# Kernel optimization log

Measured on AMD Instinct MI355X. Metric: run time of the kernel, lower is better.

## Reference

```python
import jax, jax.numpy as jnp
import numpy as np

THETA = 0.5
LEAF_SIZE = 32
N_ATOMS = 8192
N_GRAPHS = 2


def _build_tree(pos_np, indices):
    # Mirrors OpenBoundaryTreeLongRangeKernel._build_tree (octree split at bbox center).
    local = pos_np[indices]
    cmin = local.min(axis=0)
    cmax = local.max(axis=0)
    center = 0.5 * (cmin + cmax)
    half = float((cmax - cmin).max() * 0.5)
    node = {"indices": indices, "iset": set(indices), "center": center,
            "half": half, "children": [], "cid": -1}
    if len(indices) <= LEAF_SIZE:
        return node
    bins = {}
    for i in indices:
        p = pos_np[i]
        key = (int(p[0] >= center[0]), int(p[1] >= center[1]), int(p[2] >= center[2]))
        bins.setdefault(key, []).append(i)
    if len(bins) <= 1:
        return node  # degenerate split -> treated as leaf (is_leaf == no children)
    node["children"] = [_build_tree(pos_np, ci) for ci in bins.values()]
    return node


def _plan(pos_np, batch_np, n_graphs, soft):
    # Host-side Barnes-Hut traversal (the torch original does this with .item() syncs).
    # Emits flat (target, source) direct pairs and (target, cluster) monopole pairs.
    direct_t, direct_s, clus_t, clus_c = [], [], [], []
    clusters = []
    for g in range(n_graphs):
        idx = np.nonzero(batch_np == g)[0]
        if idx.size == 0:
            continue
        root = _build_tree(pos_np, [int(i) for i in idx])
        for t in idx:
            t = int(t)
            tpos = pos_np[t]
            stack = [root]
            while stack:
                node = stack.pop()
                if not node["children"]:  # leaf: direct near-field sum
                    for s in node["indices"]:
                        if s != t:
                            direct_t.append(t)
                            direct_s.append(s)
                    continue
                d = tpos - node["center"]
                dist = float(np.sqrt((d * d).sum() + soft * soft))
                diam = max(2.0 * node["half"], 1e-9)
                if (t not in node["iset"]) and (diam / dist < THETA):
                    if node["cid"] < 0:
                        node["cid"] = len(clusters)
                        clusters.append(node["indices"])
                    clus_t.append(t)
                    clus_c.append(node["cid"])
                else:
                    stack.extend(node["children"])
    if clusters:
        midx = np.concatenate([np.asarray(c, dtype=np.int32) for c in clusters])
        mseg = np.concatenate([np.full(len(c), i, np.int32) for i, c in enumerate(clusters)])
        mcnt = np.asarray([len(c) for c in clusters], dtype=np.float32)
    else:
        midx = np.zeros((0,), np.int32)
        mseg = np.zeros((0,), np.int32)
        mcnt = np.ones((1,), np.float32)
    return (np.asarray(direct_t, np.int32), np.asarray(direct_s, np.int32),
            np.asarray(clus_t, np.int32), np.asarray(clus_c, np.int32),
            midx, mseg, mcnt, max(len(clusters), 1))


def _energy(pos, source, screening, softening, plan, n_atoms):
    # Vectorized, differentiable evaluation of the planned interactions.
    dt, ds, ct, cc, midx, mseg, mcnt, n_clusters = plan
    soft2 = softening * softening
    phi = jnp.zeros((n_atoms,), dtype=pos.dtype)
    if dt.size:
        delta = pos[dt] - pos[ds]                       # [P,3]
        r = jnp.sqrt(jnp.sum(delta * delta, axis=-1) + soft2)
        phi = phi + jax.ops.segment_sum(source[ds] * jnp.exp(-screening * r) / r,
                                        dt, num_segments=n_atoms)
    if ct.size:
        q = jax.ops.segment_sum(source[midx], mseg, num_segments=n_clusters)
        center = (jax.ops.segment_sum(pos[midx], mseg, num_segments=n_clusters)
                  / jnp.asarray(mcnt)[:, None])          # differentiable cluster mean
        delta = pos[ct] - center[cc]                    # [C,3]
        r = jnp.sqrt(jnp.sum(delta * delta, axis=-1) + soft2)
        phi = phi + jax.ops.segment_sum(q[cc] * jnp.exp(-screening * r) / r,
                                        ct, num_segments=n_atoms)
    return 0.5 * (source * phi)[:, None]                # [N,1], energy_partition='potential'


def setup_inputs() -> dict:
    key = jax.random.key(0)
    k1, k2, k3 = jax.random.split(key, 3)
    pos = jax.random.normal(k1, (N_ATOMS, 3), dtype=jnp.float32) * 6.0
    batch = jnp.sort(jax.random.randint(k2, (N_ATOMS,), 0, N_GRAPHS)).astype(jnp.int32)
    cell = jnp.zeros((N_GRAPHS, 3, 3), dtype=jnp.float32)
    source = jax.random.normal(k3, (N_ATOMS,), dtype=jnp.float32)
    screening = jnp.float32(0.5)
    softening = jnp.float32(0.1)
    return {"pos": pos, "batch": batch, "cell": cell, "source": source,
            "screening": screening, "softening": softening}


def reference(pos, batch, cell, source, screening, softening):
    pos_np = np.asarray(pos, dtype=np.float32)
    batch_np = np.asarray(batch)
    plan = _plan(pos_np, batch_np, int(cell.shape[0]), float(np.asarray(softening)))
    return _energy(pos, source, screening, softening, plan, pos.shape[0])
```

## Files before the change

### kernel.cpp

```cpp
#include <hip/hip_runtime.h>

#define LEAF_SZ 32
#define MAXN 16384
#define MAXNODES 65536
#define ARENA_BASE 32768
#define MAXG 64
#define NQ 1024
#define BGRID 128
#define LCAP 256
#define LSTK 192
#define BSTK 32
#define WQCAP 64
#define NW0 16

struct __align__(64) TNode { int4 meta; float4 c4; float4 m4; float4 pad; };

__device__ int    g_perm[MAXN];
__device__ int    g_ptmp[MAXN];
__device__ float4 g_p4[MAXN];
__device__ float4 g_t4[MAXN];
__device__ int    g_nstart[MAXNODES];
__device__ int    g_nend[MAXNODES];
__device__ TNode  g_nodes[MAXNODES];
__device__ int    g_root[MAXG];
__device__ int    g_ncount;
__device__ int    g_lrange[4];
__device__ int    g_done[2];

struct NodeSh {
    float  mn[4][3], mx[4][3];
    double sx[4], sy[4], sz[4], sq[4];
    int    c8[4][8];
    int    cur[8];
    float  cc[3];
    int    info;
    int    base, num;
    int    tot[8], offk[8];
};

__device__ __forceinline__ void process_node2(NodeSh& sh, int n, int st, int en)
{
    const int tid  = threadIdx.x;
    const int wid  = tid >> 6;
    const int lane = tid & 63;
    const int cnt = en - st;

    float mnx = 3.402823466e38f, mny = mnx, mnz = mnx;
    float mxx = -mnx, mxy = -mnx, mxz = -mnx;
    double sx = 0.0, sy = 0.0, sz = 0.0, sq = 0.0;
    for (int j = st + tid; j < en; j += 256) {
        float4 p = g_p4[j];
        mnx = fminf(mnx, p.x); mny = fminf(mny, p.y); mnz = fminf(mnz, p.z);
        mxx = fmaxf(mxx, p.x); mxy = fmaxf(mxy, p.y); mxz = fmaxf(mxz, p.z);
        sx += (double)p.x; sy += (double)p.y; sz += (double)p.z; sq += (double)p.w;
    }
    for (int o = 1; o < 64; o <<= 1) {
        mnx = fminf(mnx, __shfl_xor(mnx, o));
        mny = fminf(mny, __shfl_xor(mny, o));
        mnz = fminf(mnz, __shfl_xor(mnz, o));
        mxx = fmaxf(mxx, __shfl_xor(mxx, o));
        mxy = fmaxf(mxy, __shfl_xor(mxy, o));
        mxz = fmaxf(mxz, __shfl_xor(mxz, o));
        sx += __shfl_xor(sx, o);
        sy += __shfl_xor(sy, o);
        sz += __shfl_xor(sz, o);
        sq += __shfl_xor(sq, o);
    }
    if (lane == 0) {
        sh.mn[wid][0] = mnx; sh.mn[wid][1] = mny; sh.mn[wid][2] = mnz;
        sh.mx[wid][0] = mxx; sh.mx[wid][1] = mxy; sh.mx[wid][2] = mxz;
        sh.sx[wid] = sx; sh.sy[wid] = sy; sh.sz[wid] = sz; sh.sq[wid] = sq;
    }
    __syncthreads();
    if (tid == 0) {
        float a0 = sh.mn[0][0], a1 = sh.mn[0][1], a2 = sh.mn[0][2];
        float b0 = sh.mx[0][0], b1 = sh.mx[0][1], b2 = sh.mx[0][2];
        double tx = sh.sx[0], ty = sh.sy[0], tz = sh.sz[0], tq = sh.sq[0];
        for (int w = 1; w < 4; ++w) {
            a0 = fminf(a0, sh.mn[w][0]); a1 = fminf(a1, sh.mn[w][1]); a2 = fminf(a2, sh.mn[w][2]);
            b0 = fmaxf(b0, sh.mx[w][0]); b1 = fmaxf(b1, sh.mx[w][1]); b2 = fmaxf(b2, sh.mx[w][2]);
            tx += sh.sx[w]; ty += sh.sy[w]; tz += sh.sz[w]; tq += sh.sq[w];
        }
        float cx = 0.5f * (a0 + b0), cy = 0.5f * (a1 + b1), cz = 0.5f * (a2 + b2);
        g_nodes[n].c4 = make_float4(cx, cy, cz, 0.5f * fmaxf(fmaxf(b0 - a0, b1 - a1), b2 - a2));
        const float fc = (float)cnt;
        g_nodes[n].m4 = make_float4((float)tx / fc, (float)ty / fc, (float)tz / fc, (float)tq);
        sh.cc[0] = cx; sh.cc[1] = cy; sh.cc[2] = cz;
        if (cnt <= LEAF_SZ) { g_nodes[n].meta = make_int4(st, en, 0, 0); sh.info = -1; }
        else sh.info = 0;
    }
    __syncthreads();
    if (sh.info < 0) return;
    const float cx = sh.cc[0], cy = sh.cc[1], cz = sh.cc[2];

    int c8[8] = {0,0,0,0,0,0,0,0};
    for (int j = st + tid; j < en; j += 256) {
        float4 p = g_p4[j];
        int oct = (p.x >= cx ? 1 : 0) | (p.y >= cy ? 2 : 0) | (p.z >= cz ? 4 : 0);
        c8[oct]++;
    }
    #pragma unroll
    for (int k = 0; k < 8; ++k)
        for (int o = 1; o < 64; o <<= 1)
            c8[k] += __shfl_xor(c8[k], o);
    if (lane == 0)
        #pragma unroll
        for (int k = 0; k < 8; ++k) sh.c8[wid][k] = c8[k];
    __syncthreads();
    if (tid == 0) {
        int tot[8], nonempty = 0;
        #pragma unroll
        for (int k = 0; k < 8; ++k) {
            tot[k] = sh.c8[0][k] + sh.c8[1][k] + sh.c8[2][k] + sh.c8[3][k];
            nonempty += (tot[k] > 0) ? 1 : 0;
        }
        if (nonempty <= 1) { g_nodes[n].meta = make_int4(st, en, 0, 0); sh.info = -1; }
        else {
            int base = atomicAdd(&g_ncount, nonempty);
            int acc = st, ci = base;
            #pragma unroll
            for (int k = 0; k < 8; ++k) {
                sh.cur[k] = acc;
                sh.offk[k] = acc - st;
                sh.tot[k] = tot[k];
                if (tot[k] > 0) { g_nstart[ci] = acc; g_nend[ci] = acc + tot[k]; ++ci; }
                acc += tot[k];
            }
            g_nodes[n].meta = make_int4(st, en, base, nonempty);
            sh.base = base; sh.num = nonempty; sh.info = 1;
        }
    }
    __syncthreads();
    if (sh.info < 0) return;

    for (int j = st + tid; j < en; j += 256) {
        float4 p = g_p4[j];
        int id = g_perm[j];
        int oct = (p.x >= cx ? 1 : 0) | (p.y >= cy ? 2 : 0) | (p.z >= cz ? 4 : 0);
        int pdst = atomicAdd(&sh.cur[oct], 1);
        g_ptmp[pdst] = id; g_t4[pdst] = p;
    }
    __syncthreads();
    for (int j = st + tid; j < en; j += 256) {
        g_perm[j] = g_ptmp[j];
        g_p4[j]   = g_t4[j];
    }
    __syncthreads();
}

__global__ __launch_bounds__(1024)
void level0_kernel(const float* __restrict__ pos, const float* __restrict__ src,
                   const int* __restrict__ batch, int N, int n_graphs)
{
    __shared__ int    s_first[MAXG], s_end[MAXG];
    __shared__ float  s_mn[NW0][3], s_mx[NW0][3];
    __shared__ double s_sx[NW0], s_sy[NW0], s_sz[NW0], s_sq[NW0];
    __shared__ int    s_c8[NW0][8];
    __shared__ int    s_cur[8];
    __shared__ float  s_cc[3];
    __shared__ int    s_info;
    const int tid = threadIdx.x, wid = tid >> 6, lane = tid & 63;
    const int ng = (n_graphs < MAXG) ? n_graphs : MAXG;

    for (int g = tid; g < MAXG; g += 1024) { s_first[g] = -1; s_end[g] = 0; }
    __syncthreads();
    for (int i = tid; i < N; i += 1024) {
        int b = batch[i];
        if (i == 0     || batch[i-1] != b) s_first[b] = i;
        if (i == N - 1 || batch[i+1] != b) s_end[b]   = i + 1;
    }
    __syncthreads();

    const int g = blockIdx.x;
    int nc = 0, myroot = -1;
    for (int q = 0; q < ng; ++q)
        if (s_first[q] >= 0) { if (q == g) myroot = nc; ++nc; }
    const int nb = nc + 8 * ng;

    if (g == 0 && tid == 0) {
        int r = 0;
        for (int q = 0; q < ng; ++q) {
            if (s_first[q] >= 0) g_root[q] = r++;
            else {
                g_root[q] = -1;
                for (int c = 0; c < 8; ++c) g_nstart[nc + q*8 + c] = -1;
            }
        }
        g_ncount = nb;
        g_lrange[0] = nc;
        g_lrange[1] = nb;
        g_done[1] = 0;
    }
    if (g >= ng || myroot < 0) return;

    const int st = s_first[g], en = s_end[g];
    const int cnt = en - st;
    const int n = myroot;
    const int cbase = nc + g * 8;

    float mnx = 3.402823466e38f, mny = mnx, mnz = mnx;
    float mxx = -mnx, mxy = -mnx, mxz = -mnx;
    double sx = 0.0, sy = 0.0, sz = 0.0, sq = 0.0;
    for (int j = st + tid; j < en; j += 1024) {
        float x = pos[3*j], y = pos[3*j+1], z = pos[3*j+2], s = src[j];
        mnx = fminf(mnx, x); mny = fminf(mny, y); mnz = fminf(mnz, z);
        mxx = fmaxf(mxx, x); mxy = fmaxf(mxy, y); mxz = fmaxf(mxz, z);
        sx += (double)x; sy += (double)y; sz += (double)z; sq += (double)s;
    }
    for (int o = 1; o < 64; o <<= 1) {
        mnx = fminf(mnx, __shfl_xor(mnx, o));
        mny = fminf(mny, __shfl_xor(mny, o));
        mnz = fminf(mnz, __shfl_xor(mnz, o));
        mxx = fmaxf(mxx, __shfl_xor(mxx, o));
        mxy = fmaxf(mxy, __shfl_xor(mxy, o));
        mxz = fmaxf(mxz, __shfl_xor(mxz, o));
        sx += __shfl_xor(sx, o);
        sy += __shfl_xor(sy, o);
        sz += __shfl_xor(sz, o);
        sq += __shfl_xor(sq, o);
    }
    if (lane == 0) {
        s_mn[wid][0] = mnx; s_mn[wid][1] = mny; s_mn[wid][2] = mnz;
        s_mx[wid][0] = mxx; s_mx[wid][1] = mxy; s_mx[wid][2] = mxz;
        s_sx[wid] = sx; s_sy[wid] = sy; s_sz[wid] = sz; s_sq[wid] = sq;
    }
    __syncthreads();
    if (tid == 0) {
        float a0 = s_mn[0][0], a1 = s_mn[0][1], a2 = s_mn[0][2];
        float b0 = s_mx[0][0], b1 = s_mx[0][1], b2 = s_mx[0][2];
        double tx = s_sx[0], ty = s_sy[0], tz = s_sz[0], tq = s_sq[0];
        for (int w = 1; w < NW0; ++w) {
            a0 = fminf(a0, s_mn[w][0]); a1 = fminf(a1, s_mn[w][1]); a2 = fminf(a2, s_mn[w][2]);
            b0 = fmaxf(b0, s_mx[w][0]); b1 = fmaxf(b1, s_mx[w][1]); b2 = fmaxf(b2, s_mx[w][2]);
            tx += s_sx[w]; ty += s_sy[w]; tz += s_sz[w]; tq += s_sq[w];
        }
        float cx = 0.5f * (a0 + b0), cy = 0.5f * (a1 + b1), cz = 0.5f * (a2 + b2);
        g_nodes[n].c4 = make_float4(cx, cy, cz, 0.5f * fmaxf(fmaxf(b0 - a0, b1 - a1), b2 - a2));
        const float fc = (float)cnt;
        g_nodes[n].m4 = make_float4((float)tx / fc, (float)ty / fc, (float)tz / fc, (float)tq);
        s_cc[0] = cx; s_cc[1] = cy; s_cc[2] = cz;
        s_info = (cnt <= LEAF_SZ) ? -1 : 0;
        if (s_info < 0) g_nodes[n].meta = make_int4(st, en, 0, 0);
    }
    __syncthreads();

    if (s_info == 0) {
        const float cx = s_cc[0], cy = s_cc[1], cz = s_cc[2];
        int c8[8] = {0,0,0,0,0,0,0,0};
        for (int j = st + tid; j < en; j += 1024) {
            int oct = (pos[3*j] >= cx ? 1 : 0) | (pos[3*j+1] >= cy ? 2 : 0) | (pos[3*j+2] >= cz ? 4 : 0);
            c8[oct]++;
        }
        #pragma unroll
        for (int k = 0; k < 8; ++k)
            for (int o = 1; o < 64; o <<= 1)
                c8[k] += __shfl_xor(c8[k], o);
        if (lane == 0)
            #pragma unroll
            for (int k = 0; k < 8; ++k) s_c8[wid][k] = c8[k];
        __syncthreads();
        if (tid == 0) {
            int tot[8], nonempty = 0;
            #pragma unroll
            for (int k = 0; k < 8; ++k) {
                int tk = 0;
                for (int w = 0; w < NW0; ++w) tk += s_c8[w][k];
                tot[k] = tk;
                nonempty += (tk > 0) ? 1 : 0;
            }
            if (nonempty <= 1) {
                g_nodes[n].meta = make_int4(st, en, 0, 0);
                for (int c = 0; c < 8; ++c) g_nstart[cbase + c] = -1;
                s_info = -1;
            } else {
                int acc = st, ci = cbase;
                #pragma unroll
                for (int k = 0; k < 8; ++k) {
                    s_cur[k] = acc;
                    if (tot[k] > 0) { g_nstart[ci] = acc; g_nend[ci] = acc + tot[k]; ++ci; }
                    acc += tot[k];
                }
                for (int c = ci; c < cbase + 8; ++c) g_nstart[c] = -1;
                g_nodes[n].meta = make_int4(st, en, cbase, nonempty);
                s_info = 1;
            }
        }
        __syncthreads();
    } else if (tid == 0) {
        for (int c = 0; c < 8; ++c) g_nstart[cbase + c] = -1;
    }

    if (s_info == 1) {
        const float cx = s_cc[0], cy = s_cc[1], cz = s_cc[2];
        for (int j = st + tid; j < en; j += 1024) {
            float x = pos[3*j], y = pos[3*j+1], z = pos[3*j+2], s = src[j];
            int oct = (x >= cx ? 1 : 0) | (y >= cy ? 2 : 0) | (z >= cz ? 4 : 0);
            int pdst = atomicAdd(&s_cur[oct], 1);
            g_p4[pdst] = make_float4(x, y, z, s);
            g_perm[pdst] = j;
        }
    } else {
        for (int j = st + tid; j < en; j += 1024) {
            g_p4[j] = make_float4(pos[3*j], pos[3*j+1], pos[3*j+2], src[j]);
            g_perm[j] = j;
        }
    }
}

__global__ __launch_bounds__(256) void level1_kernel()
{
    __shared__ NodeSh sh;
    const int lb = g_lrange[0], le = g_lrange[1];
    for (int n = lb + blockIdx.x; n < le; n += BGRID) {
        __syncthreads();
        int st = g_nstart[n];
        if (st < 0) continue;
        process_node2(sh, n, st, g_nend[n]);
    }
    __syncthreads();
    if (threadIdx.x == 0) {
        __threadfence();
        int d = atomicAdd(&g_done[1], 1);
        if (d == BGRID - 1)
            g_lrange[2] = atomicAdd(&g_ncount, 0);
    }
}

__device__ __forceinline__ void lds_subtree(int rootn, int st, int en, int abase,
                                            float4* a4, int* aid,
                                            int* lid, int* la, int* lbb)
{
    const int lane = threadIdx.x & 63;
    const int cnt = en - st;
    const unsigned long long mlt = (1ull << lane) - 1ull;

    for (int j = lane; j < cnt; j += 64) {
        a4[j]  = g_p4[st + j];
        aid[j] = g_perm[st + j];
    }
    asm volatile("s_waitcnt vmcnt(0) lgkmcnt(0)" ::: "memory");
    __builtin_amdgcn_wave_barrier();

    int sp = 0;
    int cn = rootn, ca = 0, cb = cnt;
    while (true) {
        const int c = cb - ca;
        float4 pv[4]; int idv[4]; int oc[4];
        float mnx = 3.402823466e38f, mny = mnx, mnz = mnx;
        float mxx = -mnx, mxy = -mnx, mxz = -mnx;
        float sx = 0.f, sy = 0.f, sz = 0.f, sq = 0.f;
        #pragma unroll
        for (int i = 0; i < 4; ++i) {
            bool act = (i*64 + lane) < c;
            int j = act ? (ca + i*64 + lane) : ca;
            float4 p = a4[j];
            pv[i] = p; idv[i] = aid[j];
            if (act) {
                mnx = fminf(mnx, p.x); mny = fminf(mny, p.y); mnz = fminf(mnz, p.z);
                mxx = fmaxf(mxx, p.x); mxy = fmaxf(mxy, p.y); mxz = fmaxf(mxz, p.z);
                sx += p.x; sy += p.y; sz += p.z; sq += p.w;
            }
        }
        for (int o = 1; o < 64; o <<= 1) {
            mnx = fminf(mnx, __shfl_xor(mnx, o));
            mny = fminf(mny, __shfl_xor(mny, o));
            mnz = fminf(mnz, __shfl_xor(mnz, o));
            mxx = fmaxf(mxx, __shfl_xor(mxx, o));
            mxy = fmaxf(mxy, __shfl_xor(mxy, o));
            mxz = fmaxf(mxz, __shfl_xor(mxz, o));
            sx += __shfl_xor(sx, o);
            sy += __shfl_xor(sy, o);
            sz += __shfl_xor(sz, o);
            sq += __shfl_xor(sq, o);
        }
        const float cx = 0.5f * (mnx + mxx);
        const float cy = 0.5f * (mny + mxy);
        const float cz = 0.5f * (mnz + mxz);
        if (lane == 0) {
            g_nodes[cn].c4 = make_float4(cx, cy, cz, 0.5f * fmaxf(fmaxf(mxx - mnx, mxy - mny), mxz - mnz));
            const float fc = (float)c;
            g_nodes[cn].m4 = make_float4(sx / fc, sy / fc, sz / fc, sq);
        }

        int nonempty = 0;
        int c8[8] = {0,0,0,0,0,0,0,0};
        if (c > LEAF_SZ) {
            #pragma unroll
            for (int i = 0; i < 4; ++i) {
                bool act = (i*64 + lane) < c;
                int o = act ? ((pv[i].x >= cx ? 1 : 0) | (pv[i].y >= cy ? 2 : 0) | (pv[i].z >= cz ? 4 : 0)) : 8;
                oc[i] = o;
                #pragma unroll
                for (int k = 0; k < 8; ++k)
                    c8[k] += (int)__popcll(__ballot(o == k));
            }
            #pragma unroll
            for (int k = 0; k < 8; ++k) nonempty += (c8[k] > 0) ? 1 : 0;
        }

        if (c <= LEAF_SZ || nonempty <= 1) {
            if (lane == 0) g_nodes[cn].meta = make_int4(st + ca, st + cb, 0, 0);
        } else {
            int off[8], acc = 0;
            #pragma unroll
            for (int k = 0; k < 8; ++k) { off[k] = acc; acc += c8[k]; }
            if (lane == 0) g_nodes[cn].meta = make_int4(st + ca, st + cb, abase, nonempty);
            int cum[8] = {0,0,0,0,0,0,0,0};
            #pragma unroll
            for (int i = 0; i < 4; ++i) {
                int o = oc[i];
                int pdst = 0;
                #pragma unroll
                for (int k = 0; k < 8; ++k) {
                    unsigned long long b = __ballot(o == k);
                    if (o == k) pdst = ca + off[k] + cum[k] + (int)__popcll(b & mlt);
                    cum[k] += (int)__popcll(b);
                }
                if (o < 8) { a4[pdst] = pv[i]; aid[pdst] = idv[i]; }
            }
            asm volatile("s_waitcnt lgkmcnt(0)" ::: "memory");
            __builtin_amdgcn_wave_barrier();
            if (lane == 0) {
                int ci = 0;
                #pragma unroll
                for (int k = 0; k < 8; ++k) {
                    if (c8[k] > 0) {
                        lid[sp + ci] = abase + ci;
                        la [sp + ci] = ca + off[k];
                        lbb[sp + ci] = ca + off[k] + c8[k];
                        ++ci;
                    }
                }
            }
            abase += nonempty; sp += nonempty;
            if (sp > LSTK) sp = LSTK;
        }
        if (sp <= 0) break;
        --sp;
        __builtin_amdgcn_wave_barrier();
        asm volatile("s_waitcnt lgkmcnt(0)" ::: "memory");
        cn = lid[sp]; ca = la[sp]; cb = lbb[sp];
        __builtin_amdgcn_wave_barrier();
    }

    for (int j = lane; j < cnt; j += 64) {
        g_p4[st + j]  = a4[j];
        g_perm[st + j] = aid[j];
    }
    asm volatile("s_waitcnt vmcnt(0)" ::: "memory");
}

__global__ __launch_bounds__(256) void block_subtree_kernel()
{
    __shared__ NodeSh sh;
    __shared__ int bs_id[BSTK], bs_st[BSTK], bs_en[BSTK];
    __shared__ int wq_id[WQCAP], wq_st[WQCAP], wq_en[WQCAP];
    __shared__ int s_bsp, s_wq;
    __shared__ float4 s_a4[4][LCAP];
    __shared__ int    s_aid[4][LCAP];
    __shared__ int    s_lid[4][LSTK], s_la[4][LSTK], s_lb[4][LSTK];

    const int tid = threadIdx.x;
    const int wid = tid >> 6;
    const int lb = g_lrange[1], le = g_lrange[2];

    for (int task = lb + blockIdx.x; task < le; task += BGRID) {
        __syncthreads();
        if (tid == 0) {
            int st = g_nstart[task], en = g_nend[task];
            if (en - st <= LCAP) { wq_id[0] = task; wq_st[0] = st; wq_en[0] = en; s_wq = 1; s_bsp = 0; }
            else                 { bs_id[0] = task; bs_st[0] = st; bs_en[0] = en; s_bsp = 1; s_wq = 0; }
        }
        __syncthreads();

        while (true) {
            __syncthreads();
            const int bsp = s_bsp;
            if (bsp == 0) break;
            const int n  = bs_id[bsp-1];
            const int st = bs_st[bsp-1];
            const int en = bs_en[bsp-1];
            __syncthreads();
            if (tid == 0) s_bsp = bsp - 1;
            process_node2(sh, n, st, en);
            if (tid == 0 && sh.info == 1) {
                int ci = 0;
                #pragma unroll
                for (int k = 0; k < 8; ++k) {
                    if (sh.tot[k] > 0) {
                        int cst = st + sh.offk[k], cen = cst + sh.tot[k];
                        int cid = sh.base + ci; ++ci;
                        if (cen - cst <= LCAP) {
                            if (s_wq < WQCAP) { wq_id[s_wq] = cid; wq_st[s_wq] = cst; wq_en[s_wq] = cen; ++s_wq; }
                        } else {
                            if (s_bsp < BSTK) { bs_id[s_bsp] = cid; bs_st[s_bsp] = cst; bs_en[s_bsp] = cen; ++s_bsp; }
                        }
                    }
                }
            }
        }
        __syncthreads();

        const int nwq = s_wq;
        float4* a4 = s_a4[wid];  int* aid = s_aid[wid];
        int* lid = s_lid[wid];   int* la = s_la[wid];  int* lbb = s_lb[wid];
        for (int i = wid; i < nwq; i += 4) {
            int cid = wq_id[i], cst = wq_st[i], cen = wq_en[i];
            lds_subtree(cid, cst, cen, ARENA_BASE + 2 * cst, a4, aid, lid, la, lbb);
        }
    }
}

__global__ __launch_bounds__(256)
void traverse_kernel(const int* __restrict__ batch,
                     const float* __restrict__ p_scr, const float* __restrict__ p_soft,
                     float* __restrict__ out, int N)
{
    __shared__ int s_q[4][NQ];
    __shared__ int s_sb[4][64], s_ss[4][64], s_mk[4][64];
    __shared__ int s_qt[4];
    const int wid  = threadIdx.x >> 6;
    const int lane = threadIdx.x & 63;
    const int slot = blockIdx.x * 4 + wid;
    if (slot >= N) return;
    const int t = g_perm[slot];

    const float scr   = p_scr[0];
    const float soft  = p_soft[0];
    const float soft2 = soft * soft;
    const float cexp  = -scr * 1.4426950408889634f;
    const float4 tp = g_p4[slot];
    const float tx = tp.x, ty = tp.y, tz = tp.z;
    const int inv_t = slot;

    volatile int* q = s_q[wid];
    int* sb = s_sb[wid];
    int* ss = s_ss[wid];
    int* mk = s_mk[wid];
    if (lane == 0) { q[0] = g_root[batch[t]]; s_qt[wid] = 1; }
    __builtin_amdgcn_wave_barrier();

    float phi = 0.f;
    int qh = 0;
    while (true) {
        __builtin_amdgcn_wave_barrier();
        int qt = ((volatile int*)s_qt)[wid];
        if (qh >= qt) break;
        int take = qt - qh; if (take > 64) take = 64;
        int node = (lane < take) ? q[(qh + lane) & (NQ - 1)] : -1;
        qh += take;

        int leaf_st = 0, leaf_cnt = 0;
        if (node >= 0) {
            const int4 meta = g_nodes[node].meta;
            if (meta.w == 0) {
                leaf_st = meta.x; leaf_cnt = meta.y - meta.x;
            } else {
                float4 c4 = g_nodes[node].c4;
                float dx = tx - c4.x, dy = ty - c4.y, dz = tz - c4.z;
                float dist = sqrtf(dx*dx + dy*dy + dz*dz + soft2);
                float diam = fmaxf(2.0f * c4.w, 1e-9f);
                bool inside = (inv_t >= meta.x) && (inv_t < meta.y);
                if (!inside && diam < 0.5f * dist) {
                    float4 m4 = g_nodes[node].m4;
                    float ax = tx - m4.x, ay = ty - m4.y, az = tz - m4.z;
                    float s = ax*ax + ay*ay + az*az + soft2;
                    float rinv = rsqrtf(s);
                    phi += m4.w * exp2f(cexp * (s * rinv)) * rinv;
                } else {
                    int p = atomicAdd(&s_qt[wid], meta.w);
                    for (int c = 0; c < meta.w; ++c) q[(p + c) & (NQ - 1)] = meta.z + c;
                }
            }
        }

        bool hasself = (inv_t >= leaf_st) && (inv_t < leaf_st + leaf_cnt);
        int cnt_adj = leaf_cnt - (hasself ? 1 : 0);
        int x = cnt_adj;
        #pragma unroll
        for (int o = 1; o < 64; o <<= 1) { int y = __shfl_up(x, o); if (lane >= o) x += y; }
        int total = __shfl(x, 63);
        int off = x - cnt_adj;

        if (total > 0) {
            sb[lane] = leaf_st - off;
            ss[lane] = hasself ? (off + (inv_t - leaf_st)) : 0x7fffffff;
            asm volatile("s_waitcnt lgkmcnt(0)" ::: "memory");
            __builtin_amdgcn_wave_barrier();
            int carry = -1;
            for (int cb = 0; cb < total; cb += 64) {
                mk[lane] = -1;
                asm volatile("s_waitcnt lgkmcnt(0)" ::: "memory");
                __builtin_amdgcn_wave_barrier();
                if (cnt_adj > 0 && off >= cb && off < cb + 64) mk[off - cb] = lane;
                asm volatile("s_waitcnt lgkmcnt(0)" ::: "memory");
                __builtin_amdgcn_wave_barrier();
                int own = mk[lane];
                if (lane == 0) own = own > carry ? own : carry;
                #pragma unroll
                for (int o = 1; o < 64; o <<= 1) {
                    int y = __shfl_up(own, o);
                    if (lane >= o) own = own > y ? own : y;
                }
                carry = __shfl(own, 63);
                int p = cb + lane;
                if (p < total) {
                    int j = sb[own] + p + ((p >= ss[own]) ? 1 : 0);
                    float4 pp = g_p4[j];
                    float dx = tx - pp.x, dy = ty - pp.y, dz = tz - pp.z;
                    float s = dx*dx + dy*dy + dz*dz + soft2;
                    float rinv = rsqrtf(s);
                    phi += pp.w * exp2f(cexp * (s * rinv)) * rinv;
                }
                __builtin_amdgcn_wave_barrier();
            }
        }
    }

    #pragma unroll
    for (int o = 1; o < 64; o <<= 1) phi += __shfl_xor(phi, o);
    if (lane == 0) out[t] = 0.5f * (tp.w * phi);
}

extern "C" void kernel_launch(void* const* d_in, const int* in_sizes, int n_in,
                              void* d_out, int out_size, void* d_ws, size_t ws_size,
                              hipStream_t stream) {
    const float* pos    = (const float*)d_in[0];
    const int*   batch  = (const int*)  d_in[1];
    const float* source = (const float*)d_in[3];
    const float* p_scr  = (const float*)d_in[4];
    const float* p_soft = (const float*)d_in[5];

    const int N        = in_sizes[0] / 3;
    const int n_graphs = in_sizes[2] / 9;

    int g0 = n_graphs > 0 ? n_graphs : 1;
    if (g0 > MAXG) g0 = MAXG;
    level0_kernel<<<g0, 1024, 0, stream>>>(pos, source, batch, N, n_graphs);
    level1_kernel<<<BGRID, 256, 0, stream>>>();
    block_subtree_kernel<<<BGRID, 256, 0, stream>>>();

    const int blocks = (N + 3) / 4;
    traverse_kernel<<<blocks, 256, 0, stream>>>(batch, p_scr, p_soft, (float*)d_out, N);
}
```

Measured before the change: 151.9 us.

## Fold level-1 node processing into block subtree kernel, dropping one launch

Removes the separate level1_kernel and its completion counter. block_subtree_kernel now takes its tasks directly from the level-1 children range and splits them itself. The block and warp queue capacities are enlarged, and a node that no longer fits the warp queue falls back to the block stack. This saves a kernel launch and a global synchronisation point, but now only up to 16 level-1 nodes (two graphs times eight) feed 128 blocks, so parallelism in the early tree build is lower.

```diff
diff --git a/kernel.cpp b/kernel.cpp
--- a/kernel.cpp
+++ b/kernel.cpp
@@ -9,8 +9,8 @@
 #define BGRID 128
 #define LCAP 256
 #define LSTK 192
-#define BSTK 32
-#define WQCAP 64
+#define BSTK 96
+#define WQCAP 256
 #define NW0 16
 
 struct __align__(64) TNode { int4 meta; float4 c4; float4 m4; float4 pad; };
@@ -25,7 +25,6 @@
 __device__ int    g_root[MAXG];
 __device__ int    g_ncount;
 __device__ int    g_lrange[4];
-__device__ int    g_done[2];
 
 struct NodeSh {
     float  mn[4][3], mx[4][3];
@@ -189,7 +188,6 @@
         g_ncount = nb;
         g_lrange[0] = nc;
         g_lrange[1] = nb;
-        g_done[1] = 0;
     }
     if (g >= ng || myroot < 0) return;
 
@@ -304,25 +302,6 @@
             g_p4[j] = make_float4(pos[3*j], pos[3*j+1], pos[3*j+2], src[j]);
             g_perm[j] = j;
         }
-    }
-}
-
-__global__ __launch_bounds__(256) void level1_kernel()
-{
-    __shared__ NodeSh sh;
-    const int lb = g_lrange[0], le = g_lrange[1];
-    for (int n = lb + blockIdx.x; n < le; n += BGRID) {
-        __syncthreads();
-        int st = g_nstart[n];
-        if (st < 0) continue;
-        process_node2(sh, n, st, g_nend[n]);
-    }
-    __syncthreads();
-    if (threadIdx.x == 0) {
-        __threadfence();
-        int d = atomicAdd(&g_done[1], 1);
-        if (d == BGRID - 1)
-            g_lrange[2] = atomicAdd(&g_ncount, 0);
     }
 }
 
@@ -462,14 +441,16 @@
 
     const int tid = threadIdx.x;
     const int wid = tid >> 6;
-    const int lb = g_lrange[1], le = g_lrange[2];
+    const int lb = g_lrange[0], le = g_lrange[1];
 
     for (int task = lb + blockIdx.x; task < le; task += BGRID) {
         __syncthreads();
+        int tst = g_nstart[task];
+        if (tst < 0) continue;
         if (tid == 0) {
-            int st = g_nstart[task], en = g_nend[task];
-            if (en - st <= LCAP) { wq_id[0] = task; wq_st[0] = st; wq_en[0] = en; s_wq = 1; s_bsp = 0; }
-            else                 { bs_id[0] = task; bs_st[0] = st; bs_en[0] = en; s_bsp = 1; s_wq = 0; }
+            int en = g_nend[task];
+            if (en - tst <= LCAP) { wq_id[0] = task; wq_st[0] = tst; wq_en[0] = en; s_wq = 1; s_bsp = 0; }
+            else                  { bs_id[0] = task; bs_st[0] = tst; bs_en[0] = en; s_bsp = 1; s_wq = 0; }
         }
         __syncthreads();
 
@@ -490,10 +471,10 @@
                     if (sh.tot[k] > 0) {
                         int cst = st + sh.offk[k], cen = cst + sh.tot[k];
                         int cid = sh.base + ci; ++ci;
-                        if (cen - cst <= LCAP) {
-                            if (s_wq < WQCAP) { wq_id[s_wq] = cid; wq_st[s_wq] = cst; wq_en[s_wq] = cen; ++s_wq; }
-                        } else {
-                            if (s_bsp < BSTK) { bs_id[s_bsp] = cid; bs_st[s_bsp] = cst; bs_en[s_bsp] = cen; ++s_bsp; }
+                        if (cen - cst <= LCAP && s_wq < WQCAP) {
+                            wq_id[s_wq] = cid; wq_st[s_wq] = cst; wq_en[s_wq] = cen; ++s_wq;
+                        } else if (s_bsp < BSTK) {
+                            bs_id[s_bsp] = cid; bs_st[s_bsp] = cst; bs_en[s_bsp] = cen; ++s_bsp;
                         }
                     }
                 }
@@ -637,7 +618,6 @@
     int g0 = n_graphs > 0 ? n_graphs : 1;
     if (g0 > MAXG) g0 = MAXG;
     level0_kernel<<<g0, 1024, 0, stream>>>(pos, source, batch, N, n_graphs);
-    level1_kernel<<<BGRID, 256, 0, stream>>>();
     block_subtree_kernel<<<BGRID, 256, 0, stream>>>();
 
     const int blocks = (N + 3) / 4;
```

Result: slower. 158.5 us (+4.4%).
